# Kernel tuning notes

Hardware: AMD Instinct MI355X
Metric: run time of the kernel (lower is better)

Reference implementation:

```python
import jax, jax.numpy as jnp
import numpy as np

# Static per-expert capacities (tokens are laid out contiguously per expert)
CAPS = [1024, 512, 1024, 256, 1024, 512, 128, 1024, 512, 1024, 256, 512, 1024, 128, 64, 512]
TOTAL = sum(CAPS)  # 9536
E, H, I = 16, 1024, 4096
OFFSETS = np.concatenate([[0], np.cumsum(CAPS)])


def setup_inputs() -> dict:
    key = jax.random.key(0)
    ks = jax.random.split(key, 5)
    x = jax.random.normal(ks[0], (TOTAL, H), dtype=jnp.float32)
    W1 = jax.random.normal(ks[1], (E, I, H), dtype=jnp.float32) * 0.02
    b1 = jax.random.normal(ks[2], (E, I), dtype=jnp.float32) * 0.02
    W2 = jax.random.normal(ks[3], (E, H, I), dtype=jnp.float32) * 0.02
    b2 = jax.random.normal(ks[4], (E, H), dtype=jnp.float32) * 0.02
    return {"x": x, "W1": W1, "b1": b1, "W2": W2, "b2": b2}


def reference(x, W1, b1, W2, b2):
    # Grouped GEMM FFN: expert e processes rows [OFFSETS[e]:OFFSETS[e+1]]
    # out = gelu(x_e @ W1[e].T + b1[e]) @ W2[e].T + b2[e]
    outs = []
    for e in range(E):  # fixed, static loop over experts (capacities are static)
        xs = x[OFFSETS[e]:OFFSETS[e + 1]]                      # [cap_e, H]
        h = jax.nn.gelu(xs @ W1[e].T + b1[e], approximate=False)  # [cap_e, I]
        outs.append(h @ W2[e].T + b2[e])                       # [cap_e, H]
    return jnp.concatenate(outs, axis=0)                       # [TOTAL, H]
```

## Files before the change

### kernel.cpp

```cpp
#include <hip/hip_runtime.h>
#include <math.h>

typedef __attribute__((ext_vector_type(8))) short short8;
typedef __attribute__((ext_vector_type(4))) float f32x4;
typedef __attribute__((ext_vector_type(2))) unsigned int u32x2;
typedef __attribute__((ext_vector_type(4))) unsigned int u32x4;

#define E_NUM 16
constexpr int CAPS[E_NUM] = {1024,512,1024,256,1024,512,128,1024,512,1024,256,512,1024,128,64,512};
constexpr int OFFS[E_NUM] = {0,1024,1536,2560,2816,3840,4352,4480,5504,6016,7040,7296,7808,8832,8960,9024};
constexpr int cdiv_(int a, int b){ return (a + b - 1) / b; }
constexpr int ilog2_(int v){ int l = 0; while ((1 << l) < v) ++l; return l; }

__device__ __forceinline__ unsigned int cvt_pk_bf16(float a, float b){
  unsigned int r;
  asm("v_cvt_pk_bf16_f32 %0, %1, %2" : "=v"(r) : "v"(a), "v"(b));
  return r;
}

typedef __attribute__((address_space(1))) const unsigned char gas_u8;
typedef __attribute__((address_space(3))) unsigned char las_u8;
__device__ __forceinline__ void gl_lds16(const void* g, void* l){
  __builtin_amdgcn_global_load_lds((gas_u8*)g, (las_u8*)l, 16, 0, 0);
}

__global__ __launch_bounds__(256) void cvt_bf16_kernel(const float* __restrict__ x,
                                                       unsigned short* __restrict__ xb, int n8)
{
  int i = blockIdx.x * blockDim.x + threadIdx.x;
  const int stride = gridDim.x * blockDim.x;
  for (; i < n8; i += stride) {
    f32x4 a = *reinterpret_cast<const f32x4*>(x + (size_t)i * 8);
    f32x4 b = *reinterpret_cast<const f32x4*>(x + (size_t)i * 8 + 4);
    u32x2 lo, hi;
    lo[0] = cvt_pk_bf16(a[0], a[1]); lo[1] = cvt_pk_bf16(a[2], a[3]);
    hi[0] = cvt_pk_bf16(b[0], b[1]); hi[1] = cvt_pk_bf16(b[2], b[3]);
    *reinterpret_cast<u32x2*>(xb + (size_t)i * 8)     = lo;
    *reinterpret_cast<u32x2*>(xb + (size_t)i * 8 + 4) = hi;
  }
}

template<int NDIM, int KDIM, int LOG_GN, int NWG>
__global__ __launch_bounds__(512, 2)
void g1_gemm256(const unsigned short* __restrict__ Ah, const float* __restrict__ W,
                const float* __restrict__ bias, unsigned short* __restrict__ Oh)
{
  constexpr int A_BYTES = 256 * 64;
  constexpr int B_BYTES = 256 * 128;
  constexpr int BUF  = A_BYTES + B_BYTES;
  constexpr int GN   = 1 << LOG_GN;
  constexpr int NTT  = KDIM / 32;
  static_assert(NWG % 8 == 0);
  static_assert(NTT >= 3);

  __shared__ __align__(16) char smem[3 * BUF];

  const int tid  = threadIdx.x;
  const int braw = blockIdx.x;
  const int tt = (braw & 7) * (NWG / 8) + (braw >> 3);

  int m0 = 0, n0 = 0, Me = 0, tok0 = 0;
  size_t wbase = 0, bbase = 0;
  {
    int acc0 = 0;
    #pragma unroll
    for (int i = 0; i < E_NUM; ++i) {
      const int mt  = cdiv_(CAPS[i], 256);
      const int lmt = ilog2_(mt);
      const int nb  = mt * (NDIM / 256);
      if (tt >= acc0 && tt < acc0 + nb) {
        const int loc = tt - acc0;
        const int g   = loc >> (lmt + LOG_GN);
        const int rem = loc & ((mt << LOG_GN) - 1);
        m0   = (rem >> LOG_GN) * 256;
        n0   = ((g << LOG_GN) | (rem & (GN - 1))) * 256;
        Me   = CAPS[i];
        tok0 = OFFS[i];
        wbase = (size_t)i * NDIM * KDIM;
        bbase = (size_t)i * NDIM;
      }
      acc0 += nb;
    }
  }
  const float* Wb = W + wbase;

  const int lane = tid & 63;
  const int wv   = tid >> 6;

  auto stageA = [&](int buf, int kt) {
    const unsigned short* Ag = Ah + (size_t)(tok0 + m0) * KDIM + kt * 32;
    char* dst0 = smem + buf * BUF;
    #pragma unroll
    for (int j = 0; j < 2; ++j) {
      const int rbase = j * 128 + wv * 16;
      const int r     = rbase + (lane >> 2);
      const int blk   = (lane & 3) ^ (r & 3);
      gl_lds16((const void*)(Ag + (size_t)r * KDIM + blk * 8), (void*)(dst0 + rbase * 64));
    }
  };
  auto stageB = [&](int buf, int kt) {
    const float* Bg = Wb + (size_t)n0 * KDIM + kt * 32;
    char* dst0 = smem + buf * BUF + A_BYTES;
    #pragma unroll
    for (int j = 0; j < 4; ++j) {
      const int rbase = j * 64 + wv * 8;
      const int r     = rbase + (lane >> 3);
      const int blk   = (lane & 7) ^ (r & 7);
      gl_lds16((const void*)(Bg + (size_t)r * KDIM + blk * 4), (void*)(dst0 + rbase * 128));
    }
  };

  const int wm   = (wv >> 2) * 128;
  const int wn   = (wv & 3) * 64;
  const int lrow = lane & 15;
  const int pa0  = (((lane >> 4) ^ (lane & 3)) << 4);
  const int pb0  = ((((lane >> 4) << 1) ^ (lane & 7)) << 4);

  f32x4 acc_[8][4];
  #pragma unroll
  for (int i = 0; i < 8; ++i)
    #pragma unroll
    for (int j = 0; j < 4; ++j)
      acc_[i][j] = (f32x4){0.f, 0.f, 0.f, 0.f};

  auto compute = [&](int cur) {
    const char* ab  = smem + cur * BUF;
    const char* bbp = smem + cur * BUF + A_BYTES;
    short8 bfr[4];
    #pragma unroll
    for (int f = 0; f < 4; ++f) {
      const char* rowp = bbp + (size_t)(wn + f * 16 + lrow) * 128;
      f32x4 lo = *reinterpret_cast<const f32x4*>(rowp + pb0);
      f32x4 hi = *reinterpret_cast<const f32x4*>(rowp + (pb0 ^ 16));
      u32x4 pk;
      pk[0] = cvt_pk_bf16(lo[0], lo[1]); pk[1] = cvt_pk_bf16(lo[2], lo[3]);
      pk[2] = cvt_pk_bf16(hi[0], hi[1]); pk[3] = cvt_pk_bf16(hi[2], hi[3]);
      bfr[f] = __builtin_bit_cast(short8, pk);
    }
    #pragma unroll
    for (int i = 0; i < 8; ++i) {
      short8 afr = *reinterpret_cast<const short8*>(ab + (wm + i * 16 + lrow) * 64 + pa0);
      #pragma unroll
      for (int j = 0; j < 4; ++j)
        acc_[i][j] = __builtin_amdgcn_mfma_f32_16x16x32_bf16(afr, bfr[j], acc_[i][j], 0, 0, 0);
    }
  };

  stageA(0, 0); stageB(0, 0);
  stageA(1, 1); stageB(1, 1);
  int cur = 0, nx2 = 2;
  for (int kt = 0; kt < NTT; ++kt) {
    if (kt + 1 < NTT) asm volatile("s_waitcnt vmcnt(6)\n\ts_barrier" ::: "memory");
    else              asm volatile("s_waitcnt vmcnt(0)\n\ts_barrier" ::: "memory");
    __builtin_amdgcn_sched_barrier(0);
    if (kt + 2 < NTT) { stageA(nx2, kt + 2); stageB(nx2, kt + 2); }
    compute(cur);
    cur = (cur == 2) ? 0 : cur + 1;
    nx2 = (nx2 == 2) ? 0 : nx2 + 1;
  }

  float bv[4];
  #pragma unroll
  for (int f = 0; f < 4; ++f)
    bv[f] = bias[bbase + n0 + wn + f * 16 + lrow];

  __syncthreads();
  unsigned short* hout = (unsigned short*)smem;
  #pragma unroll
  for (int i = 0; i < 8; ++i) {
    const int rbase = wm + i * 16 + (lane >> 4) * 4;
    #pragma unroll
    for (int j = 0; j < 4; ++j) {
      #pragma unroll
      for (int jj = 0; jj < 4; ++jj) {
        float xv = acc_[i][j][jj] + bv[j];
        float y2 = xv * (1.5957691216057308f + 0.07135481627f * xv * xv);
        float g  = xv * __builtin_amdgcn_rcpf(1.0f + __expf(-y2));
        hout[(rbase + jj) * 256 + wn + j * 16 + lrow] = (unsigned short)(cvt_pk_bf16(g, g) & 0xFFFFu);
      }
    }
  }
  __syncthreads();
  #pragma unroll
  for (int s = 0; s < 16; ++s) {
    const int row = s * 16 + (tid >> 5);
    const int c   = (tid & 31) * 8;
    if (m0 + row < Me) {
      *reinterpret_cast<short8*>(Oh + (size_t)(tok0 + m0 + row) * NDIM + n0 + c)
        = *reinterpret_cast<const short8*>(hout + row * 256 + c);
    }
  }
}

template<int NDIM, int KDIM, int NWG>
__global__ __launch_bounds__(256, 3)
void g2_gemm128c(const unsigned short* __restrict__ Ah, const unsigned short* __restrict__ Wh,
                 const float* __restrict__ bias, float* __restrict__ Of)
{
  constexpr int T_BYTES = 128 * 64;
  constexpr int BUF  = 2 * T_BYTES;
  constexpr int NT   = KDIM / 32;
  static_assert(NWG % 8 == 0);
  static_assert(NT >= 3);

  __shared__ __align__(16) char smem[3 * BUF];

  const int tid  = threadIdx.x;
  const int braw = blockIdx.x;
  const int tt = (braw & 7) * (NWG / 8) + (braw >> 3);

  int m0 = 0, n0 = 0, Me = 0, tok0 = 0;
  size_t wbase = 0, bbase = 0;
  {
    int acc0 = 0;
    #pragma unroll
    for (int i = 0; i < E_NUM; ++i) {
      const int mt = cdiv_(CAPS[i], 128);
      const int nb = mt * (NDIM / 128);
      if (tt >= acc0 && tt < acc0 + nb) {
        const int loc = tt - acc0;
        m0   = (loc & (mt - 1)) * 128;
        n0   = (loc >> ilog2_(mt)) * 128;
        Me   = CAPS[i];
        tok0 = OFFS[i];
        wbase = (size_t)i * NDIM * KDIM;
        bbase = (size_t)i * NDIM;
      }
      acc0 += nb;
    }
  }

  const int lane = tid & 63;
  const int wv   = tid >> 6;
  const int wm   = (wv >> 1) * 64;
  const int wn   = (wv & 1) * 64;
  const int lrow = lane & 15;
  const int pa0  = (((lane >> 4) ^ (lane & 3)) << 4);

  const unsigned short* Abase = Ah + (size_t)(tok0 + m0) * KDIM;
  const unsigned short* Bbase = Wh + wbase + (size_t)n0 * KDIM;

  auto stage_tile = [&](const unsigned short* base, char* dst0, int kt) {
    const unsigned short* Tg = base + kt * 32;
    #pragma unroll
    for (int j = 0; j < 2; ++j) {
      const int rbase = wv * 32 + j * 16;
      const int r     = rbase + (lane >> 2);
      const int blk   = (lane & 3) ^ (r & 3);
      gl_lds16((const void*)(Tg + (size_t)r * KDIM + blk * 8), (void*)(dst0 + rbase * 64));
    }
  };
  auto stage = [&](int buf, int kt) {
    stage_tile(Abase, smem + buf * BUF, kt);
    stage_tile(Bbase, smem + buf * BUF + T_BYTES, kt);
  };

  f32x4 acc_[4][4];
  #pragma unroll
  for (int i = 0; i < 4; ++i)
    #pragma unroll
    for (int j = 0; j < 4; ++j)
      acc_[i][j] = (f32x4){0.f, 0.f, 0.f, 0.f};

  auto compute = [&](int cur) {
    const char* ab = smem + cur * BUF;
    const char* bb = smem + cur * BUF + T_BYTES;
    short8 afr[4], bfr[4];
    #pragma unroll
    for (int f = 0; f < 4; ++f)
      afr[f] = *reinterpret_cast<const short8*>(ab + (wm + f * 16 + lrow) * 64 + pa0);
    #pragma unroll
    for (int f = 0; f < 4; ++f)
      bfr[f] = *reinterpret_cast<const short8*>(bb + (wn + f * 16 + lrow) * 64 + pa0);
    #pragma unroll
    for (int i = 0; i < 4; ++i)
      #pragma unroll
      for (int j = 0; j < 4; ++j)
        acc_[i][j] = __builtin_amdgcn_mfma_f32_16x16x32_bf16(afr[i], bfr[j], acc_[i][j], 0, 0, 0);
  };

  stage(0, 0);
  stage(1, 1);
  int cur = 0, nx2 = 2;
  for (int kt = 0; kt < NT; ++kt) {
    if (kt + 1 < NT) asm volatile("s_waitcnt vmcnt(4)\n\ts_barrier" ::: "memory");
    else             asm volatile("s_waitcnt vmcnt(0)\n\ts_barrier" ::: "memory");
    __builtin_amdgcn_sched_barrier(0);
    if (kt + 2 < NT) stage(nx2, kt + 2);
    compute(cur);
    cur = (cur == 2) ? 0 : cur + 1;
    nx2 = (nx2 == 2) ? 0 : nx2 + 1;
  }

  float bv[4];
  #pragma unroll
  for (int f = 0; f < 4; ++f)
    bv[f] = bias[bbase + n0 + wn + f * 16 + lrow];

  #pragma unroll
  for (int i = 0; i < 4; ++i) {
    const int rbase = wm + i * 16 + (lane >> 4) * 4;
    #pragma unroll
    for (int jj = 0; jj < 4; ++jj) {
      int grow = m0 + rbase + jj;
      if (grow < Me) {
        #pragma unroll
        for (int j = 0; j < 4; ++j) {
          Of[(size_t)(tok0 + grow) * NDIM + n0 + wn + j * 16 + lrow] = acc_[i][j][jj] + bv[j];
        }
      }
    }
  }
}

extern "C" void kernel_launch(void* const* d_in, const int* in_sizes, int n_in,
                              void* d_out, int out_size, void* d_ws, size_t ws_size,
                              hipStream_t stream)
{
  const float* x  = (const float*)d_in[0];
  const float* W1 = (const float*)d_in[1];
  const float* b1 = (const float*)d_in[2];
  const float* W2 = (const float*)d_in[3];
  const float* b2 = (const float*)d_in[4];
  float* out = (float*)d_out;

  constexpr size_t H_BYTES   = (size_t)9536 * 4096 * 2;
  constexpr size_t XB_BYTES  = (size_t)9536 * 1024 * 2;
  unsigned short* h   = (unsigned short*)d_ws;
  unsigned short* xb  = (unsigned short*)((char*)d_ws + H_BYTES);
  unsigned short* w2b = (unsigned short*)((char*)d_ws + H_BYTES + XB_BYTES);

  cvt_bf16_kernel<<<2048, 256, 0, stream>>>(x, xb, 9536 * 1024 / 8);

  g1_gemm256<4096, 1024, 2, 624><<<624, 512, 0, stream>>>(xb, W1, b1, h);

  cvt_bf16_kernel<<<2048, 256, 0, stream>>>(W2, w2b, 16 * 1024 * 4096 / 8);

  g2_gemm128c<1024, 4096, 600><<<600, 256, 0, stream>>>(h, w2b, b2, out);
}
```

Before: 358.5 us.

## Pre-convert W1 to bf16 and reuse the 128-tile GEMM with fused GELU

Drops the specialized 256x256 first-layer GEMM, which loaded fp32 W1 tiles and converted them to bf16 inside its inner loop. W1 is now converted to bf16 in a separate pass. The first layer then runs on the generic 128x128 bf16 GEMM, templated to fuse bias, GELU and a staged bf16 store. This costs an extra full read and write of W1 plus a larger workspace, and smaller tiles mean less operand reuse, in exchange for a simpler inner loop with higher occupancy.

```diff
diff --git a/kernel.cpp b/kernel.cpp
--- a/kernel.cpp
+++ b/kernel.cpp
@@ -4,7 +4,6 @@
 typedef __attribute__((ext_vector_type(8))) short short8;
 typedef __attribute__((ext_vector_type(4))) float f32x4;
 typedef __attribute__((ext_vector_type(2))) unsigned int u32x2;
-typedef __attribute__((ext_vector_type(4))) unsigned int u32x4;
 
 #define E_NUM 16
 constexpr int CAPS[E_NUM] = {1024,512,1024,256,1024,512,128,1024,512,1024,256,512,1024,128,64,512};
@@ -40,162 +39,10 @@
   }
 }
 
-template<int NDIM, int KDIM, int LOG_GN, int NWG>
-__global__ __launch_bounds__(512, 2)
-void g1_gemm256(const unsigned short* __restrict__ Ah, const float* __restrict__ W,
-                const float* __restrict__ bias, unsigned short* __restrict__ Oh)
-{
-  constexpr int A_BYTES = 256 * 64;
-  constexpr int B_BYTES = 256 * 128;
-  constexpr int BUF  = A_BYTES + B_BYTES;
-  constexpr int GN   = 1 << LOG_GN;
-  constexpr int NTT  = KDIM / 32;
-  static_assert(NWG % 8 == 0);
-  static_assert(NTT >= 3);
-
-  __shared__ __align__(16) char smem[3 * BUF];
-
-  const int tid  = threadIdx.x;
-  const int braw = blockIdx.x;
-  const int tt = (braw & 7) * (NWG / 8) + (braw >> 3);
-
-  int m0 = 0, n0 = 0, Me = 0, tok0 = 0;
-  size_t wbase = 0, bbase = 0;
-  {
-    int acc0 = 0;
-    #pragma unroll
-    for (int i = 0; i < E_NUM; ++i) {
-      const int mt  = cdiv_(CAPS[i], 256);
-      const int lmt = ilog2_(mt);
-      const int nb  = mt * (NDIM / 256);
-      if (tt >= acc0 && tt < acc0 + nb) {
-        const int loc = tt - acc0;
-        const int g   = loc >> (lmt + LOG_GN);
-        const int rem = loc & ((mt << LOG_GN) - 1);
-        m0   = (rem >> LOG_GN) * 256;
-        n0   = ((g << LOG_GN) | (rem & (GN - 1))) * 256;
-        Me   = CAPS[i];
-        tok0 = OFFS[i];
-        wbase = (size_t)i * NDIM * KDIM;
-        bbase = (size_t)i * NDIM;
-      }
-      acc0 += nb;
-    }
-  }
-  const float* Wb = W + wbase;
-
-  const int lane = tid & 63;
-  const int wv   = tid >> 6;
-
-  auto stageA = [&](int buf, int kt) {
-    const unsigned short* Ag = Ah + (size_t)(tok0 + m0) * KDIM + kt * 32;
-    char* dst0 = smem + buf * BUF;
-    #pragma unroll
-    for (int j = 0; j < 2; ++j) {
-      const int rbase = j * 128 + wv * 16;
-      const int r     = rbase + (lane >> 2);
-      const int blk   = (lane & 3) ^ (r & 3);
-      gl_lds16((const void*)(Ag + (size_t)r * KDIM + blk * 8), (void*)(dst0 + rbase * 64));
-    }
-  };
-  auto stageB = [&](int buf, int kt) {
-    const float* Bg = Wb + (size_t)n0 * KDIM + kt * 32;
-    char* dst0 = smem + buf * BUF + A_BYTES;
-    #pragma unroll
-    for (int j = 0; j < 4; ++j) {
-      const int rbase = j * 64 + wv * 8;
-      const int r     = rbase + (lane >> 3);
-      const int blk   = (lane & 7) ^ (r & 7);
-      gl_lds16((const void*)(Bg + (size_t)r * KDIM + blk * 4), (void*)(dst0 + rbase * 128));
-    }
-  };
-
-  const int wm   = (wv >> 2) * 128;
-  const int wn   = (wv & 3) * 64;
-  const int lrow = lane & 15;
-  const int pa0  = (((lane >> 4) ^ (lane & 3)) << 4);
-  const int pb0  = ((((lane >> 4) << 1) ^ (lane & 7)) << 4);
-
-  f32x4 acc_[8][4];
-  #pragma unroll
-  for (int i = 0; i < 8; ++i)
-    #pragma unroll
-    for (int j = 0; j < 4; ++j)
-      acc_[i][j] = (f32x4){0.f, 0.f, 0.f, 0.f};
-
-  auto compute = [&](int cur) {
-    const char* ab  = smem + cur * BUF;
-    const char* bbp = smem + cur * BUF + A_BYTES;
-    short8 bfr[4];
-    #pragma unroll
-    for (int f = 0; f < 4; ++f) {
-      const char* rowp = bbp + (size_t)(wn + f * 16 + lrow) * 128;
-      f32x4 lo = *reinterpret_cast<const f32x4*>(rowp + pb0);
-      f32x4 hi = *reinterpret_cast<const f32x4*>(rowp + (pb0 ^ 16));
-      u32x4 pk;
-      pk[0] = cvt_pk_bf16(lo[0], lo[1]); pk[1] = cvt_pk_bf16(lo[2], lo[3]);
-      pk[2] = cvt_pk_bf16(hi[0], hi[1]); pk[3] = cvt_pk_bf16(hi[2], hi[3]);
-      bfr[f] = __builtin_bit_cast(short8, pk);
-    }
-    #pragma unroll
-    for (int i = 0; i < 8; ++i) {
-      short8 afr = *reinterpret_cast<const short8*>(ab + (wm + i * 16 + lrow) * 64 + pa0);
-      #pragma unroll
-      for (int j = 0; j < 4; ++j)
-        acc_[i][j] = __builtin_amdgcn_mfma_f32_16x16x32_bf16(afr, bfr[j], acc_[i][j], 0, 0, 0);
-    }
-  };
-
-  stageA(0, 0); stageB(0, 0);
-  stageA(1, 1); stageB(1, 1);
-  int cur = 0, nx2 = 2;
-  for (int kt = 0; kt < NTT; ++kt) {
-    if (kt + 1 < NTT) asm volatile("s_waitcnt vmcnt(6)\n\ts_barrier" ::: "memory");
-    else              asm volatile("s_waitcnt vmcnt(0)\n\ts_barrier" ::: "memory");
-    __builtin_amdgcn_sched_barrier(0);
-    if (kt + 2 < NTT) { stageA(nx2, kt + 2); stageB(nx2, kt + 2); }
-    compute(cur);
-    cur = (cur == 2) ? 0 : cur + 1;
-    nx2 = (nx2 == 2) ? 0 : nx2 + 1;
-  }
-
-  float bv[4];
-  #pragma unroll
-  for (int f = 0; f < 4; ++f)
-    bv[f] = bias[bbase + n0 + wn + f * 16 + lrow];
-
-  __syncthreads();
-  unsigned short* hout = (unsigned short*)smem;
-  #pragma unroll
-  for (int i = 0; i < 8; ++i) {
-    const int rbase = wm + i * 16 + (lane >> 4) * 4;
-    #pragma unroll
-    for (int j = 0; j < 4; ++j) {
-      #pragma unroll
-      for (int jj = 0; jj < 4; ++jj) {
-        float xv = acc_[i][j][jj] + bv[j];
-        float y2 = xv * (1.5957691216057308f + 0.07135481627f * xv * xv);
-        float g  = xv * __builtin_amdgcn_rcpf(1.0f + __expf(-y2));
-        hout[(rbase + jj) * 256 + wn + j * 16 + lrow] = (unsigned short)(cvt_pk_bf16(g, g) & 0xFFFFu);
-      }
-    }
-  }
-  __syncthreads();
-  #pragma unroll
-  for (int s = 0; s < 16; ++s) {
-    const int row = s * 16 + (tid >> 5);
-    const int c   = (tid & 31) * 8;
-    if (m0 + row < Me) {
-      *reinterpret_cast<short8*>(Oh + (size_t)(tok0 + m0 + row) * NDIM + n0 + c)
-        = *reinterpret_cast<const short8*>(hout + row * 256 + c);
-    }
-  }
-}
-
-template<int NDIM, int KDIM, int NWG>
+template<bool GELU_OUT, int NDIM, int KDIM, int NWG>
 __global__ __launch_bounds__(256, 3)
-void g2_gemm128c(const unsigned short* __restrict__ Ah, const unsigned short* __restrict__ Wh,
-                 const float* __restrict__ bias, float* __restrict__ Of)
+void gemm128_bf16(const unsigned short* __restrict__ Ah, const unsigned short* __restrict__ Wh,
+                  const float* __restrict__ bias, void* __restrict__ Outv)
 {
   constexpr int T_BYTES = 128 * 64;
   constexpr int BUF  = 2 * T_BYTES;
@@ -297,16 +144,48 @@
   for (int f = 0; f < 4; ++f)
     bv[f] = bias[bbase + n0 + wn + f * 16 + lrow];
 
-  #pragma unroll
-  for (int i = 0; i < 4; ++i) {
-    const int rbase = wm + i * 16 + (lane >> 4) * 4;
-    #pragma unroll
-    for (int jj = 0; jj < 4; ++jj) {
-      int grow = m0 + rbase + jj;
+  if constexpr (GELU_OUT) {
+    unsigned short* Oh = (unsigned short*)Outv;
+    __syncthreads();
+    unsigned short* hout = (unsigned short*)smem;
+    #pragma unroll
+    for (int i = 0; i < 4; ++i) {
+      const int rbase = wm + i * 16 + (lane >> 4) * 4;
+      #pragma unroll
+      for (int j = 0; j < 4; ++j) {
+        #pragma unroll
+        for (int jj = 0; jj < 4; ++jj) {
+          float xv = acc_[i][j][jj] + bv[j];
+          float y2 = xv * (1.5957691216057308f + 0.07135481627f * xv * xv);
+          float g  = xv * __builtin_amdgcn_rcpf(1.0f + __expf(-y2));
+          hout[(rbase + jj) * 128 + wn + j * 16 + lrow] = (unsigned short)(cvt_pk_bf16(g, g) & 0xFFFFu);
+        }
+      }
+    }
+    __syncthreads();
+    #pragma unroll
+    for (int it = 0; it < 8; ++it) {
+      int row  = it * 16 + (tid >> 4);
+      int c    = (tid & 15) * 8;
+      int grow = m0 + row;
       if (grow < Me) {
-        #pragma unroll
-        for (int j = 0; j < 4; ++j) {
-          Of[(size_t)(tok0 + grow) * NDIM + n0 + wn + j * 16 + lrow] = acc_[i][j][jj] + bv[j];
+        *reinterpret_cast<short8*>(Oh + (size_t)(tok0 + grow) * NDIM + n0 + c)
+          = *reinterpret_cast<const short8*>(hout + row * 128 + c);
+      }
+    }
+  } else {
+    float* Of = (float*)Outv;
+    #pragma unroll
+    for (int i = 0; i < 4; ++i) {
+      const int rbase = wm + i * 16 + (lane >> 4) * 4;
+      #pragma unroll
+      for (int jj = 0; jj < 4; ++jj) {
+        int grow = m0 + rbase + jj;
+        if (grow < Me) {
+          #pragma unroll
+          for (int j = 0; j < 4; ++j) {
+            Of[(size_t)(tok0 + grow) * NDIM + n0 + wn + j * 16 + lrow] = acc_[i][j][jj] + bv[j];
+          }
         }
       }
     }
@@ -326,15 +205,19 @@
 
   constexpr size_t H_BYTES   = (size_t)9536 * 4096 * 2;
   constexpr size_t XB_BYTES  = (size_t)9536 * 1024 * 2;
+  constexpr size_t W1B_BYTES = (size_t)16 * 4096 * 1024 * 2;
   unsigned short* h   = (unsigned short*)d_ws;
   unsigned short* xb  = (unsigned short*)((char*)d_ws + H_BYTES);
-  unsigned short* w2b = (unsigned short*)((char*)d_ws + H_BYTES + XB_BYTES);
+  unsigned short* w1b = (unsigned short*)((char*)d_ws + H_BYTES + XB_BYTES);
+  unsigned short* w2b = (unsigned short*)((char*)d_ws + H_BYTES + XB_BYTES + W1B_BYTES);
 
   cvt_bf16_kernel<<<2048, 256, 0, stream>>>(x, xb, 9536 * 1024 / 8);
 
-  g1_gemm256<4096, 1024, 2, 624><<<624, 512, 0, stream>>>(xb, W1, b1, h);
+  cvt_bf16_kernel<<<2048, 256, 0, stream>>>(W1, w1b, 16 * 4096 * 1024 / 8);
+
+  gemm128_bf16<true, 4096, 1024, 2400><<<2400, 256, 0, stream>>>(xb, w1b, b1, (void*)h);
 
   cvt_bf16_kernel<<<2048, 256, 0, stream>>>(W2, w2b, 16 * 1024 * 4096 / 8);
 
-  g2_gemm128c<1024, 4096, 600><<<600, 256, 0, stream>>>(h, w2b, b2, out);
-}
+  gemm128_bf16<false, 1024, 4096, 600><<<600, 256, 0, stream>>>(h, w2b, b2, (void*)out);
+}
```

New measurement: 391.3 us. 1.09x slower.
